# Kernel tuning notes

Measured on AMD Instinct MI355X. Metric: run time of the kernel, lower is better.

The kernel has to match this reference:

```python
import jax, jax.numpy as jnp
import numpy as np

VOCAB = 50000
EMB = 128
ENC = 128
B = 256
K = 4            # tree arity
DEPTH = 5        # root at depth 0
N_NODES = (K ** (DEPTH + 1) - 1) // (K - 1)  # 1365, BFS order: children of i are K*i+1..K*i+K


def setup_inputs() -> dict:
    key = jax.random.key(0)
    ks = jax.random.split(key, 9)
    s = 0.05
    return {
        "tokens": jax.random.randint(ks[0], (N_NODES, B), 0, VOCAB, dtype=jnp.int32),
        "emb_table": jax.random.normal(ks[1], (VOCAB, EMB), jnp.float32) * s,
        "W_ih": jax.random.normal(ks[2], (3 * ENC, EMB), jnp.float32) * s,
        "W_hh": jax.random.normal(ks[3], (3 * ENC, ENC), jnp.float32) * s,
        "b_ih": jax.random.normal(ks[4], (3 * ENC,), jnp.float32) * s,
        "b_hh": jax.random.normal(ks[5], (3 * ENC,), jnp.float32) * s,
        "sent_weight": jax.random.normal(ks[6], (ENC, ENC), jnp.float32) * s,
        "sent_bias": jax.random.normal(ks[7], (1, ENC), jnp.float32) * s,
        "context_weight": jax.random.normal(ks[8], (ENC, 1), jnp.float32) * s,
    }


def _gru_step(x, h, W_ih, W_hh, b_ih, b_hh):
    # torch.nn.GRU single step: gates ordered (r, z, n)
    gi = x @ W_ih.T + b_ih
    gh = h @ W_hh.T + b_hh
    i_r, i_z, i_n = jnp.split(gi, 3, axis=-1)
    h_r, h_z, h_n = jnp.split(gh, 3, axis=-1)
    r = jax.nn.sigmoid(i_r + h_r)
    z = jax.nn.sigmoid(i_z + h_z)
    n = jnp.tanh(i_n + r * h_n)
    return (1.0 - z) * n + z * h


def _encode(tokens, emb_table, W_ih, W_hh, b_ih, b_hh, sent_weight, sent_bias, context_weight):
    # bottom-up over levels of a full K-ary tree; vectorized over (nodes-in-level, batch)
    level_starts = [(K ** d - 1) // (K - 1) for d in range(DEPTH + 2)]
    bsz = tokens.shape[1]
    outs = []
    child_h = None  # [n_{d+1}, B, ENC] hiddens of the level below, level-local order
    for d in range(DEPTH, -1, -1):
        s, e = level_starts[d], level_starts[d + 1]
        n_d = e - s
        x = emb_table[tokens[s:e]]  # [n_d, B, EMB]
        if child_h is None:
            h0 = jnp.zeros((n_d, bsz, ENC), x.dtype)  # leaves: no children
        else:
            # children of local node j are rows j*K..j*K+K-1 of child_h
            ch = child_h.reshape(n_d, K, bsz, ENC).transpose(1, 0, 2, 3)  # [K, n_d, B, E]
            u = jnp.tanh(jnp.einsum('knbe,ef->knbf', ch, sent_weight) + sent_bias)
            scores = jnp.tanh(jnp.einsum('knbe,eo->knbo', u, context_weight))[..., 0]  # [K, n_d, B]
            alpha = jax.nn.softmax(scores, axis=0)  # softmax over children, per (node, batch)
            h0 = jnp.einsum('knbe,knb->nbe', ch, alpha)
        hn = _gru_step(x, h0, W_ih, W_hh, b_ih, b_hh)  # [n_d, B, E]
        outs.append(hn)
        child_h = hn
    all_h = jnp.concatenate(outs, axis=0)  # [N_NODES, B, E]
    return jnp.max(all_h, axis=0)  # torch.max(node_list, 0)[0]


def reference(tokens, emb_table, W_ih, W_hh, b_ih, b_hh, sent_weight, sent_bias, context_weight):
    return _encode(tokens, emb_table, W_ih, W_hh, b_ih, b_hh,
                   sent_weight, sent_bias, context_weight)
```

## Files before the change

### kernel.cpp

```cpp
#include <hip/hip_runtime.h>
#include <hip/hip_bf16.h>
#include <math.h>

typedef short s8 __attribute__((ext_vector_type(8)));
typedef float f4 __attribute__((ext_vector_type(4)));
typedef unsigned short ushort_t;

__device__ __forceinline__ float fexp2f(float x) { return __builtin_amdgcn_exp2f(x); }
__device__ __forceinline__ float frcpf(float x)  { return __builtin_amdgcn_rcpf(x); }
__device__ __forceinline__ float sigf(float x) {
    return frcpf(1.f + fexp2f(x * -1.44269504f));
}
__device__ __forceinline__ float tanh_f(float x) {
    float e = fexp2f(x * 2.88539008f);
    return 1.f - 2.f * frcpf(e + 1.f);
}
__device__ __forceinline__ unsigned pk2(float a, float b) {
    __hip_bfloat162 r = __float22bfloat162_rn(make_float2(a, b));
    return *(unsigned*)&r;
}
__device__ __forceinline__ float b2f(ushort_t b) {
    return __uint_as_float(((unsigned)b) << 16);
}

#define EMB_N   6400000
#define W_N     49152
#define SW_N    16384
#define CVT_N   (EMB_N + 2 * W_N + SW_N)

__global__ __launch_bounds__(256) void cvt_kernel(
    const float* __restrict__ emb, const float* __restrict__ wih,
    const float* __restrict__ whh, const float* __restrict__ sw,
    ushort_t* __restrict__ embb, ushort_t* __restrict__ wihb,
    ushort_t* __restrict__ whhb, ushort_t* __restrict__ swtb)
{
    int i = (blockIdx.x * 256 + threadIdx.x) * 4;
    if (i >= CVT_N) return;
    if (i < EMB_N) {
        float4 v = *(const float4*)(emb + i);
        uint2 o; o.x = pk2(v.x, v.y); o.y = pk2(v.z, v.w);
        *(uint2*)(embb + i) = o;
    } else if (i < EMB_N + W_N) {
        int j = i - EMB_N;
        float4 v = *(const float4*)(wih + j);
        uint2 o; o.x = pk2(v.x, v.y); o.y = pk2(v.z, v.w);
        *(uint2*)(wihb + j) = o;
    } else if (i < EMB_N + 2 * W_N) {
        int j = i - EMB_N - W_N;
        float4 v = *(const float4*)(whh + j);
        uint2 o; o.x = pk2(v.x, v.y); o.y = pk2(v.z, v.w);
        *(uint2*)(whhb + j) = o;
    } else {
        int j = i - EMB_N - 2 * W_N;
        int f = j >> 7, e0 = j & 127;
        uint2 o;
        o.x = pk2(sw[(e0 + 0) * 128 + f], sw[(e0 + 1) * 128 + f]);
        o.y = pk2(sw[(e0 + 2) * 128 + f], sw[(e0 + 3) * 128 + f]);
        *(uint2*)(swtb + j) = o;
    }
}

__global__ __launch_bounds__(512, 2) void leafgru_mfma(
    const ushort_t* __restrict__ embb, const ushort_t* __restrict__ wihb,
    const float* __restrict__ bih, const float* __restrict__ bhh,
    const ushort_t* __restrict__ swt, const float* __restrict__ sb,
    const float* __restrict__ cw,
    ushort_t* __restrict__ hleaf, float* __restrict__ sleaf)
{
    __shared__ ushort_t xs[128 * 136];
    __shared__ ushort_t hnew[128 * 136];
    __shared__ float scp[8][128];

    const int t = threadIdx.x;
    const int base = blockIdx.x * 128;

    {
        int lr = t >> 2, c0 = (t & 3) * 32;
        const ushort_t* src = embb + (size_t)(base + lr) * 128 + c0;
        ushort_t* dst = &xs[lr * 136 + c0];
        #pragma unroll
        for (int i = 0; i < 4; ++i) *(s8*)(dst + 8 * i) = *(const s8*)(src + 8 * i);
    }

    const int lane = t & 63, w = t >> 6;
    const int quad = lane >> 4, l15 = lane & 15;
    const int gA = w * 16 + l15;
    const int g0 = w * 16 + quad * 4;

    s8 bwi[3][4];
    #pragma unroll
    for (int gm = 0; gm < 3; ++gm) {
        const ushort_t* wp = wihb + (size_t)(gm * 128 + gA) * 128 + quad * 8;
        #pragma unroll
        for (int s = 0; s < 4; ++s) bwi[gm][s] = *(const s8*)(wp + 32 * s);
    }
    float bR[4], bZ[4], biN[4], bhN[4];
    {
        float4 a = *(const float4*)(bih + g0);
        float4 b = *(const float4*)(bhh + g0);
        bR[0] = a.x + b.x; bR[1] = a.y + b.y; bR[2] = a.z + b.z; bR[3] = a.w + b.w;
        float4 c = *(const float4*)(bih + 128 + g0);
        float4 d = *(const float4*)(bhh + 128 + g0);
        bZ[0] = c.x + d.x; bZ[1] = c.y + d.y; bZ[2] = c.z + d.z; bZ[3] = c.w + d.w;
        float4 e = *(const float4*)(bih + 256 + g0);
        float4 f = *(const float4*)(bhh + 256 + g0);
        biN[0] = e.x; biN[1] = e.y; biN[2] = e.z; biN[3] = e.w;
        bhN[0] = f.x; bhN[1] = f.y; bhN[2] = f.z; bhN[3] = f.w;
    }

    __syncthreads();

    #pragma unroll 1
    for (int mt = 0; mt < 8; ++mt) {
        const int row = mt * 16 + l15;
        s8 ax[4];
        const ushort_t* ap = &xs[row * 136 + quad * 8];
        #pragma unroll
        for (int s = 0; s < 4; ++s) ax[s] = *(const s8*)(ap + 32 * s);

        f4 accR = (f4)0.f, accZ = (f4)0.f, accN = (f4)0.f;
        #pragma unroll
        for (int s = 0; s < 4; ++s) {
            accR = __builtin_amdgcn_mfma_f32_16x16x32_bf16(bwi[0][s], ax[s], accR, 0, 0, 0);
            accZ = __builtin_amdgcn_mfma_f32_16x16x32_bf16(bwi[1][s], ax[s], accZ, 0, 0, 0);
            accN = __builtin_amdgcn_mfma_f32_16x16x32_bf16(bwi[2][s], ax[s], accN, 0, 0, 0);
        }
        float hv[4];
        #pragma unroll
        for (int r = 0; r < 4; ++r) {
            float G = fexp2f((accR[r] + bR[r]) * -1.44269504f);
            float rr = frcpf(1.f + G);
            float an = accN[r] + biN[r] + rr * bhN[r];
            float E = fexp2f(an * 2.88539008f);
            float F = fexp2f((accZ[r] + bZ[r]) * -1.44269504f);
            float d = frcpf((E + 1.f) * (1.f + F));
            hv[r] = (E - 1.f) * F * d;
        }
        uint2 ov; ov.x = pk2(hv[0], hv[1]); ov.y = pk2(hv[2], hv[3]);
        *(uint2*)&hnew[row * 136 + g0] = ov;
        *(uint2*)(hleaf + (size_t)(base + row) * 128 + g0) = ov;
    }
    __syncthreads();

    s8 bsw[4];
    {
        const ushort_t* wp = swt + (size_t)gA * 128 + quad * 8;
        #pragma unroll
        for (int s = 0; s < 4; ++s) bsw[s] = *(const s8*)(wp + 32 * s);
    }
    float sb4[4], cw4[4];
    {
        float4 a = *(const float4*)(sb + g0);
        float4 b = *(const float4*)(cw + g0);
        sb4[0] = a.x; sb4[1] = a.y; sb4[2] = a.z; sb4[3] = a.w;
        cw4[0] = b.x; cw4[1] = b.y; cw4[2] = b.z; cw4[3] = b.w;
    }

    #pragma unroll 1
    for (int mt = 0; mt < 8; ++mt) {
        const int crow = mt * 16 + l15;
        s8 a[4];
        const ushort_t* ap = &hnew[crow * 136 + quad * 8];
        #pragma unroll
        for (int s = 0; s < 4; ++s) a[s] = *(const s8*)(ap + 32 * s);

        f4 acc = (f4)0.f;
        #pragma unroll
        for (int s = 0; s < 4; ++s)
            acc = __builtin_amdgcn_mfma_f32_16x16x32_bf16(bsw[s], a[s], acc, 0, 0, 0);

        float part = 0.f;
        #pragma unroll
        for (int r = 0; r < 4; ++r)
            part += tanh_f(acc[r] + sb4[r]) * cw4[r];
        part += __shfl_xor(part, 16);
        part += __shfl_xor(part, 32);
        if (quad == 0) scp[w][crow] = part;
    }
    __syncthreads();

    if (t < 128) {
        float s = 0.f;
        #pragma unroll
        for (int ww = 0; ww < 8; ++ww) s += scp[ww][t];
        sleaf[base + t] = tanh_f(s);
    }
}

__global__ __launch_bounds__(512, 2) void gru_fused(
    const int* __restrict__ tokens, const ushort_t* __restrict__ embb,
    const ushort_t* __restrict__ hleaf, const float* __restrict__ sleaf,
    const ushort_t* __restrict__ wihb, const ushort_t* __restrict__ whhb,
    const float* __restrict__ bih, const float* __restrict__ bhh,
    ushort_t* __restrict__ hbuf, ushort_t* __restrict__ pmaxs)
{
    __shared__ ushort_t xs[128 * 136];
    __shared__ ushort_t hs[128 * 136];

    const int t = threadIdx.x;
    const int base = blockIdx.x * 128;

    {
        int rl = t >> 2, c0 = (t & 3) * 32;
        int row = base + rl;
        int node = row >> 8, b = row & 255;
        int tok = tokens[(85 + node) * 256 + b];
        const ushort_t* src = embb + (size_t)tok * 128 + c0;
        ushort_t* dst = &xs[rl * 136 + c0];
        #pragma unroll
        for (int i = 0; i < 4; ++i) *(s8*)(dst + 8 * i) = *(const s8*)(src + 8 * i);

        int lt0 = tokens[(341 + 4 * node + 0) * 256 + b];
        int lt1 = tokens[(341 + 4 * node + 1) * 256 + b];
        int lt2 = tokens[(341 + 4 * node + 2) * 256 + b];
        int lt3 = tokens[(341 + 4 * node + 3) * 256 + b];
        float s0 = sleaf[lt0], s1 = sleaf[lt1], s2 = sleaf[lt2], s3 = sleaf[lt3];
        float m = fmaxf(fmaxf(s0, s1), fmaxf(s2, s3));
        float e0 = fexp2f((s0 - m) * 1.44269504f), e1 = fexp2f((s1 - m) * 1.44269504f);
        float e2 = fexp2f((s2 - m) * 1.44269504f), e3 = fexp2f((s3 - m) * 1.44269504f);
        float inv = frcpf(e0 + e1 + e2 + e3);
        float a0 = e0 * inv, a1 = e1 * inv, a2 = e2 * inv, a3 = e3 * inv;

        const ushort_t* p0 = hleaf + (size_t)lt0 * 128 + c0;
        const ushort_t* p1 = hleaf + (size_t)lt1 * 128 + c0;
        const ushort_t* p2 = hleaf + (size_t)lt2 * 128 + c0;
        const ushort_t* p3 = hleaf + (size_t)lt3 * 128 + c0;
        ushort_t* hdst = &hs[rl * 136 + c0];
        ushort_t* pmp = pmaxs + ((size_t)b * 320 + node) * 128 + c0;
        #pragma unroll
        for (int i = 0; i < 4; ++i) {
            s8 v0 = *(const s8*)(p0 + 8 * i);
            s8 v1 = *(const s8*)(p1 + 8 * i);
            s8 v2 = *(const s8*)(p2 + 8 * i);
            s8 v3 = *(const s8*)(p3 + 8 * i);
            float o[8], mm[8];
            #pragma unroll
            for (int j = 0; j < 8; ++j) {
                float x0 = b2f((ushort_t)v0[j]), x1 = b2f((ushort_t)v1[j]);
                float x2 = b2f((ushort_t)v2[j]), x3 = b2f((ushort_t)v3[j]);
                o[j]  = a0 * x0 + a1 * x1 + a2 * x2 + a3 * x3;
                mm[j] = fmaxf(fmaxf(x0, x1), fmaxf(x2, x3));
            }
            uint4 ovv, mvv;
            ovv.x = pk2(o[0], o[1]);  ovv.y = pk2(o[2], o[3]);
            ovv.z = pk2(o[4], o[5]);  ovv.w = pk2(o[6], o[7]);
            mvv.x = pk2(mm[0], mm[1]); mvv.y = pk2(mm[2], mm[3]);
            mvv.z = pk2(mm[4], mm[5]); mvv.w = pk2(mm[6], mm[7]);
            *(uint4*)(hdst + 8 * i) = ovv;
            *(uint4*)(pmp + 8 * i)  = mvv;
        }
    }

    const int lane = t & 63, w = t >> 6;
    const int quad = lane >> 4, l15 = lane & 15;
    const int gA = w * 16 + l15;
    const int g0 = w * 16 + quad * 4;

    s8 bwi[3][4], bwh[3][4];
    #pragma unroll
    for (int gm = 0; gm < 3; ++gm) {
        const ushort_t* wp = wihb + (size_t)(gm * 128 + gA) * 128 + quad * 8;
        #pragma unroll
        for (int s = 0; s < 4; ++s) bwi[gm][s] = *(const s8*)(wp + 32 * s);
        const ushort_t* wp2 = whhb + (size_t)(gm * 128 + gA) * 128 + quad * 8;
        #pragma unroll
        for (int s = 0; s < 4; ++s) bwh[gm][s] = *(const s8*)(wp2 + 32 * s);
    }

    float bR[4], bZ[4], biN[4], bhN[4];
    {
        float4 a = *(const float4*)(bih + g0);
        float4 b = *(const float4*)(bhh + g0);
        bR[0] = a.x + b.x; bR[1] = a.y + b.y; bR[2] = a.z + b.z; bR[3] = a.w + b.w;
        float4 c = *(const float4*)(bih + 128 + g0);
        float4 d = *(const float4*)(bhh + 128 + g0);
        bZ[0] = c.x + d.x; bZ[1] = c.y + d.y; bZ[2] = c.z + d.z; bZ[3] = c.w + d.w;
        float4 e = *(const float4*)(bih + 256 + g0);
        float4 f = *(const float4*)(bhh + 256 + g0);
        biN[0] = e.x; biN[1] = e.y; biN[2] = e.z; biN[3] = e.w;
        bhN[0] = f.x; bhN[1] = f.y; bhN[2] = f.z; bhN[3] = f.w;
    }

    __syncthreads();

    #pragma unroll 1
    for (int mt = 0; mt < 8; ++mt) {
        const int row = mt * 16 + l15;
        s8 ax[4], ah[4];
        {
            const ushort_t* ap = &xs[row * 136 + quad * 8];
            #pragma unroll
            for (int s = 0; s < 4; ++s) ax[s] = *(const s8*)(ap + 32 * s);
            const ushort_t* hp = &hs[row * 136 + quad * 8];
            #pragma unroll
            for (int s = 0; s < 4; ++s) ah[s] = *(const s8*)(hp + 32 * s);
        }

        f4 accR = (f4)0.f, accZ = (f4)0.f, accN = (f4)0.f, accNh = (f4)0.f;
        #pragma unroll
        for (int s = 0; s < 4; ++s) {
            accR = __builtin_amdgcn_mfma_f32_16x16x32_bf16(bwi[0][s], ax[s], accR, 0, 0, 0);
            accZ = __builtin_amdgcn_mfma_f32_16x16x32_bf16(bwi[1][s], ax[s], accZ, 0, 0, 0);
            accN = __builtin_amdgcn_mfma_f32_16x16x32_bf16(bwi[2][s], ax[s], accN, 0, 0, 0);
        }
        #pragma unroll
        for (int s = 0; s < 4; ++s) {
            accR  = __builtin_amdgcn_mfma_f32_16x16x32_bf16(bwh[0][s], ah[s], accR, 0, 0, 0);
            accZ  = __builtin_amdgcn_mfma_f32_16x16x32_bf16(bwh[1][s], ah[s], accZ, 0, 0, 0);
            accNh = __builtin_amdgcn_mfma_f32_16x16x32_bf16(bwh[2][s], ah[s], accNh, 0, 0, 0);
        }

        float h0v[4];
        {
            short4 h04 = *(const short4*)&hs[row * 136 + g0];
            h0v[0] = b2f((ushort_t)h04.x); h0v[1] = b2f((ushort_t)h04.y);
            h0v[2] = b2f((ushort_t)h04.z); h0v[3] = b2f((ushort_t)h04.w);
        }
        float hv[4];
        #pragma unroll
        for (int r = 0; r < 4; ++r) {
            float G = fexp2f((accR[r] + bR[r]) * -1.44269504f);
            float rr = frcpf(1.f + G);
            float an = accN[r] + biN[r] + rr * (accNh[r] + bhN[r]);
            float E = fexp2f(an * 2.88539008f);
            float F = fexp2f((accZ[r] + bZ[r]) * -1.44269504f);
            float d = frcpf((E + 1.f) * (1.f + F));
            hv[r] = ((E - 1.f) * F + h0v[r] * (E + 1.f)) * d;
        }
        uint2 ov; ov.x = pk2(hv[0], hv[1]); ov.y = pk2(hv[2], hv[3]);
        *(uint2*)(hbuf + (size_t)(base + row) * 128 + g0) = ov;
    }
}

__global__ __launch_bounds__(512, 2) void attnmax_mfma(
    const ushort_t* __restrict__ hch, ushort_t* __restrict__ h0out,
    ushort_t* __restrict__ pmax,
    const ushort_t* __restrict__ swt, const float* __restrict__ sb,
    const float* __restrict__ cw)
{
    __shared__ ushort_t chs[128 * 136];
    __shared__ float scp[8][128];
    __shared__ float sc[128];
    __shared__ float al[4][32];

    const int t = threadIdx.x;
    const int pbase = blockIdx.x * 32;
    const int pnode = pbase >> 8;
    const int b0 = pbase & 255;

    {
        int lr = t >> 2, c0 = (t & 3) * 32;
        int k = lr >> 5, bl = lr & 31;
        const ushort_t* src = hch + ((size_t)(4 * pnode + k) * 256 + b0 + bl) * 128 + c0;
        ushort_t* dst = &chs[lr * 136 + c0];
        #pragma unroll
        for (int i = 0; i < 4; ++i) *(s8*)(dst + 8 * i) = *(const s8*)(src + 8 * i);
    }

    const int lane = t & 63, w = t >> 6;
    const int quad = lane >> 4, l15 = lane & 15;
    const int fA = w * 16 + l15;
    const int f0 = w * 16 + quad * 4;

    s8 bsw[4];
    {
        const ushort_t* wp = swt + (size_t)fA * 128 + quad * 8;
        #pragma unroll
        for (int s = 0; s < 4; ++s) bsw[s] = *(const s8*)(wp + 32 * s);
    }
    float sb4[4], cw4[4];
    {
        float4 a = *(const float4*)(sb + f0);
        float4 b = *(const float4*)(cw + f0);
        sb4[0] = a.x; sb4[1] = a.y; sb4[2] = a.z; sb4[3] = a.w;
        cw4[0] = b.x; cw4[1] = b.y; cw4[2] = b.z; cw4[3] = b.w;
    }
    __syncthreads();

    #pragma unroll 1
    for (int mt = 0; mt < 8; ++mt) {
        const int crow = mt * 16 + l15;
        s8 a[4];
        const ushort_t* ap = &chs[crow * 136 + quad * 8];
        #pragma unroll
        for (int s = 0; s < 4; ++s) a[s] = *(const s8*)(ap + 32 * s);

        f4 acc = (f4)0.f;
        #pragma unroll
        for (int s = 0; s < 4; ++s)
            acc = __builtin_amdgcn_mfma_f32_16x16x32_bf16(bsw[s], a[s], acc, 0, 0, 0);

        float part = 0.f;
        #pragma unroll
        for (int r = 0; r < 4; ++r)
            part += tanh_f(acc[r] + sb4[r]) * cw4[r];
        part += __shfl_xor(part, 16);
        part += __shfl_xor(part, 32);
        if (quad == 0) scp[w][crow] = part;
    }
    __syncthreads();

    if (t < 128) {
        float s = 0.f;
        #pragma unroll
        for (int ww = 0; ww < 8; ++ww) s += scp[ww][t];
        sc[t] = tanh_f(s);
    }
    __syncthreads();

    if (t < 32) {
        float s0 = sc[t], s1 = sc[32 + t], s2 = sc[64 + t], s3 = sc[96 + t];
        float m = fmaxf(fmaxf(s0, s1), fmaxf(s2, s3));
        float e0 = fexp2f((s0 - m) * 1.44269504f), e1 = fexp2f((s1 - m) * 1.44269504f);
        float e2 = fexp2f((s2 - m) * 1.44269504f), e3 = fexp2f((s3 - m) * 1.44269504f);
        float inv = frcpf(e0 + e1 + e2 + e3);
        al[0][t] = e0 * inv; al[1][t] = e1 * inv; al[2][t] = e2 * inv; al[3][t] = e3 * inv;
    }
    __syncthreads();

    {
        int bl = t >> 4, e0 = (t & 15) * 8;
        float a0 = al[0][bl], a1 = al[1][bl], a2 = al[2][bl], a3 = al[3][bl];
        s8 c0v = *(const s8*)&chs[(0 * 32 + bl) * 136 + e0];
        s8 c1v = *(const s8*)&chs[(1 * 32 + bl) * 136 + e0];
        s8 c2v = *(const s8*)&chs[(2 * 32 + bl) * 136 + e0];
        s8 c3v = *(const s8*)&chs[(3 * 32 + bl) * 136 + e0];
        float o[8], m[8];
        #pragma unroll
        for (int j = 0; j < 8; ++j) {
            float x0 = b2f((ushort_t)c0v[j]), x1 = b2f((ushort_t)c1v[j]);
            float x2 = b2f((ushort_t)c2v[j]), x3 = b2f((ushort_t)c3v[j]);
            o[j] = a0 * x0 + a1 * x1 + a2 * x2 + a3 * x3;
            m[j] = fmaxf(fmaxf(x0, x1), fmaxf(x2, x3));
        }
        uint4 ovv, mvv;
        ovv.x = pk2(o[0], o[1]); ovv.y = pk2(o[2], o[3]);
        ovv.z = pk2(o[4], o[5]); ovv.w = pk2(o[6], o[7]);
        mvv.x = pk2(m[0], m[1]); mvv.y = pk2(m[2], m[3]);
        mvv.z = pk2(m[4], m[5]); mvv.w = pk2(m[6], m[7]);
        size_t rh = ((size_t)pnode * 256 + b0 + bl) * 128 + e0;
        *(uint4*)(h0out + rh) = ovv;
        size_t rp = ((size_t)(b0 + bl) * 320 + 256 + pnode) * 128 + e0;
        *(uint4*)(pmax + rp) = mvv;
    }
}

__global__ __launch_bounds__(512, 1) void tail_kernel(
    const int* __restrict__ tokens, const ushort_t* __restrict__ embb,
    const ushort_t* __restrict__ wihb, const ushort_t* __restrict__ whhb,
    const float* __restrict__ bih, const float* __restrict__ bhh,
    const ushort_t* __restrict__ swt, const float* __restrict__ sb,
    const float* __restrict__ cw,
    const ushort_t* __restrict__ h0g,
    const ushort_t* __restrict__ pmax,
    float* __restrict__ out)
{
    __shared__ ushort_t xs[64 * 136];
    __shared__ ushort_t hnew[64 * 136];
    __shared__ ushort_t hs[64 * 136];
    __shared__ float scp[8][64];
    __shared__ float sc[64];
    __shared__ float al[4][16];
    __shared__ float smax[4][128];
    __shared__ float wpart[8][128];

    const int t = threadIdx.x;
    const int bb = blockIdx.x;
    const int lane = t & 63, w = t >> 6;
    const int quad = lane >> 4, l15 = lane & 15;
    const int gA = w * 16 + l15;
    const int g0 = w * 16 + quad * 4;

    s8 bwi[3][4], bwh[3][4];
    #pragma unroll
    for (int gm = 0; gm < 3; ++gm) {
        const ushort_t* wp = wihb + (size_t)(gm * 128 + gA) * 128 + quad * 8;
        #pragma unroll
        for (int s = 0; s < 4; ++s) bwi[gm][s] = *(const s8*)(wp + 32 * s);
        const ushort_t* wp2 = whhb + (size_t)(gm * 128 + gA) * 128 + quad * 8;
        #pragma unroll
        for (int s = 0; s < 4; ++s) bwh[gm][s] = *(const s8*)(wp2 + 32 * s);
    }
    float bR[4], bZ[4], biN[4], bhN[4];
    {
        float4 a = *(const float4*)(bih + g0);
        float4 b = *(const float4*)(bhh + g0);
        bR[0] = a.x + b.x; bR[1] = a.y + b.y; bR[2] = a.z + b.z; bR[3] = a.w + b.w;
        float4 c = *(const float4*)(bih + 128 + g0);
        float4 d = *(const float4*)(bhh + 128 + g0);
        bZ[0] = c.x + d.x; bZ[1] = c.y + d.y; bZ[2] = c.z + d.z; bZ[3] = c.w + d.w;
        float4 e = *(const float4*)(bih + 256 + g0);
        float4 f = *(const float4*)(bhh + 256 + g0);
        biN[0] = e.x; biN[1] = e.y; biN[2] = e.z; biN[3] = e.w;
        bhN[0] = f.x; bhN[1] = f.y; bhN[2] = f.z; bhN[3] = f.w;
    }
    s8 bsw[4];
    {
        const ushort_t* wp = swt + (size_t)gA * 128 + quad * 8;
        #pragma unroll
        for (int s = 0; s < 4; ++s) bsw[s] = *(const s8*)(wp + 32 * s);
    }
    float sb4[4], cw4[4];
    {
        float4 a = *(const float4*)(sb + g0);
        float4 b = *(const float4*)(cw + g0);
        sb4[0] = a.x; sb4[1] = a.y; sb4[2] = a.z; sb4[3] = a.w;
        cw4[0] = b.x; cw4[1] = b.y; cw4[2] = b.z; cw4[3] = b.w;
    }

    float vmax = -INFINITY;

    const int nodesA[4] = {64, 16, 4, 1};
    const int tok0A[4]  = {21, 5, 1, 0};

    #pragma unroll 1
    for (int L = 0; L < 4; ++L) {
        const int nodes = nodesA[L], tok0 = tok0A[L];
        const int R = (nodes < 16) ? 16 : nodes;
        const int mts = R >> 4;

        {
            int lr = t >> 3, c0 = (t & 7) * 16;
            if (lr < R) {
                int n = min(lr, nodes - 1);
                int tok = tokens[(tok0 + n) * 256 + bb];
                const ushort_t* src = embb + (size_t)tok * 128 + c0;
                ushort_t* dst = &xs[lr * 136 + c0];
                *(s8*)(dst)     = *(const s8*)(src);
                *(s8*)(dst + 8) = *(const s8*)(src + 8);
                if (L == 0) {
                    const ushort_t* hsrc = h0g + ((size_t)n * 256 + bb) * 128 + c0;
                    ushort_t* hdst = &hs[lr * 136 + c0];
                    *(s8*)(hdst)     = *(const s8*)(hsrc);
                    *(s8*)(hdst + 8) = *(const s8*)(hsrc + 8);
                }
            }
        }
        __syncthreads();

        for (int mt = 0; mt < mts; ++mt) {
            const int row = mt * 16 + l15;
            const int hr = min(row, nodes - 1);
            s8 ax[4], ah[4];
            {
                const ushort_t* ap = &xs[row * 136 + quad * 8];
                #pragma unroll
                for (int s = 0; s < 4; ++s) ax[s] = *(const s8*)(ap + 32 * s);
                const ushort_t* hp = &hs[hr * 136 + quad * 8];
                #pragma unroll
                for (int s = 0; s < 4; ++s) ah[s] = *(const s8*)(hp + 32 * s);
            }
            f4 accR = (f4)0.f, accZ = (f4)0.f, accN = (f4)0.f, accNh = (f4)0.f;
            #pragma unroll
            for (int s = 0; s < 4; ++s) {
                accR = __builtin_amdgcn_mfma_f32_16x16x32_bf16(bwi[0][s], ax[s], accR, 0, 0, 0);
                accZ = __builtin_amdgcn_mfma_f32_16x16x32_bf16(bwi[1][s], ax[s], accZ, 0, 0, 0);
                accN = __builtin_amdgcn_mfma_f32_16x16x32_bf16(bwi[2][s], ax[s], accN, 0, 0, 0);
            }
            #pragma unroll
            for (int s = 0; s < 4; ++s) {
                accR  = __builtin_amdgcn_mfma_f32_16x16x32_bf16(bwh[0][s], ah[s], accR, 0, 0, 0);
                accZ  = __builtin_amdgcn_mfma_f32_16x16x32_bf16(bwh[1][s], ah[s], accZ, 0, 0, 0);
                accNh = __builtin_amdgcn_mfma_f32_16x16x32_bf16(bwh[2][s], ah[s], accNh, 0, 0, 0);
            }
            float h0v[4];
            {
                short4 h04 = *(const short4*)&hs[hr * 136 + g0];
                h0v[0] = b2f((ushort_t)h04.x); h0v[1] = b2f((ushort_t)h04.y);
                h0v[2] = b2f((ushort_t)h04.z); h0v[3] = b2f((ushort_t)h04.w);
            }
            float hv[4];
            #pragma unroll
            for (int r = 0; r < 4; ++r) {
                float rr = sigf(accR[r] + bR[r]);
                float zz = sigf(accZ[r] + bZ[r]);
                float nn = tanh_f(accN[r] + biN[r] + rr * (accNh[r] + bhN[r]));
                hv[r] = nn + zz * (h0v[r] - nn);
            }
            uint2 ov; ov.x = pk2(hv[0], hv[1]); ov.y = pk2(hv[2], hv[3]);
            *(uint2*)&hnew[row * 136 + g0] = ov;
        }
        __syncthreads();

        {
            int col = t & 127, g = t >> 7;
            for (int r = g; r < R; r += 4)
                vmax = fmaxf(vmax, b2f(hnew[r * 136 + col]));
        }

        if (L < 3) {
            for (int mt = 0; mt < mts; ++mt) {
                const int crow = mt * 16 + l15;
                s8 a[4];
                const ushort_t* ap = &hnew[crow * 136 + quad * 8];
                #pragma unroll
                for (int s = 0; s < 4; ++s) a[s] = *(const s8*)(ap + 32 * s);
                f4 acc = (f4)0.f;
                #pragma unroll
                for (int s = 0; s < 4; ++s)
                    acc = __builtin_amdgcn_mfma_f32_16x16x32_bf16(bsw[s], a[s], acc, 0, 0, 0);
                float part = 0.f;
                #pragma unroll
                for (int r = 0; r < 4; ++r)
                    part += tanh_f(acc[r] + sb4[r]) * cw4[r];
                part += __shfl_xor(part, 16);
                part += __shfl_xor(part, 32);
                if (quad == 0) scp[w][crow] = part;
            }
            __syncthreads();
            if (t < R) {
                float s = 0.f;
                #pragma unroll
                for (int g = 0; g < 8; ++g) s += scp[g][t];
                sc[t] = tanh_f(s);
            }
            __syncthreads();
            const int P = nodes >> 2;
            if (t < P) {
                float s0 = sc[4 * t + 0], s1 = sc[4 * t + 1];
                float s2 = sc[4 * t + 2], s3 = sc[4 * t + 3];
                float m = fmaxf(fmaxf(s0, s1), fmaxf(s2, s3));
                float e0 = fexp2f((s0 - m) * 1.44269504f);
                float e1 = fexp2f((s1 - m) * 1.44269504f);
                float e2 = fexp2f((s2 - m) * 1.44269504f);
                float e3 = fexp2f((s3 - m) * 1.44269504f);
                float inv = frcpf(e0 + e1 + e2 + e3);
                al[0][t] = e0 * inv; al[1][t] = e1 * inv;
                al[2][t] = e2 * inv; al[3][t] = e3 * inv;
            }
            __syncthreads();
            if (t < 16 * P) {
                int bl = t >> 4, e0 = (t & 15) * 8;
                float a0 = al[0][bl], a1 = al[1][bl], a2 = al[2][bl], a3 = al[3][bl];
                s8 c0v = *(const s8*)&hnew[(4 * bl + 0) * 136 + e0];
                s8 c1v = *(const s8*)&hnew[(4 * bl + 1) * 136 + e0];
                s8 c2v = *(const s8*)&hnew[(4 * bl + 2) * 136 + e0];
                s8 c3v = *(const s8*)&hnew[(4 * bl + 3) * 136 + e0];
                float o[8];
                #pragma unroll
                for (int j = 0; j < 8; ++j) {
                    o[j] = a0 * b2f((ushort_t)c0v[j]) + a1 * b2f((ushort_t)c1v[j])
                         + a2 * b2f((ushort_t)c2v[j]) + a3 * b2f((ushort_t)c3v[j]);
                }
                uint4 ovv;
                ovv.x = pk2(o[0], o[1]); ovv.y = pk2(o[2], o[3]);
                ovv.z = pk2(o[4], o[5]); ovv.w = pk2(o[6], o[7]);
                *(uint4*)&hs[bl * 136 + e0] = ovv;
            }
            __syncthreads();
        }
    }

    smax[t >> 7][t & 127] = vmax;

    {
        int cg = t & 15;
        int ck = t >> 4;
        const ushort_t* base = pmax + (size_t)bb * 320 * 128 + cg * 8;
        float v8[8];
        #pragma unroll
        for (int j = 0; j < 8; ++j) v8[j] = -INFINITY;
        for (int s = ck; s < 320; s += 32) {
            s8 c = *(const s8*)(base + (size_t)s * 128);
            #pragma unroll
            for (int j = 0; j < 8; ++j) v8[j] = fmaxf(v8[j], b2f((ushort_t)c[j]));
        }
        #pragma unroll
        for (int j = 0; j < 8; ++j) {
            v8[j] = fmaxf(v8[j], __shfl_xor(v8[j], 16));
            v8[j] = fmaxf(v8[j], __shfl_xor(v8[j], 32));
        }
        if (lane < 16) {
            #pragma unroll
            for (int j = 0; j < 8; ++j) wpart[w][lane * 8 + j] = v8[j];
        }
    }
    __syncthreads();

    if (t < 128) {
        float m = wpart[0][t];
        #pragma unroll
        for (int ww = 1; ww < 8; ++ww) m = fmaxf(m, wpart[ww][t]);
        float own = fmaxf(fmaxf(smax[0][t], smax[1][t]),
                          fmaxf(smax[2][t], smax[3][t]));
        out[(size_t)bb * 128 + t] = fmaxf(m, own);
    }
}

extern "C" void kernel_launch(void* const* d_in, const int* in_sizes, int n_in,
                              void* d_out, int out_size, void* d_ws, size_t ws_size,
                              hipStream_t stream)
{
    const int*   tokens = (const int*)d_in[0];
    const float* emb    = (const float*)d_in[1];
    const float* Wih    = (const float*)d_in[2];
    const float* Whh    = (const float*)d_in[3];
    const float* bih    = (const float*)d_in[4];
    const float* bhh    = (const float*)d_in[5];
    const float* SW     = (const float*)d_in[6];
    const float* sb     = (const float*)d_in[7];
    const float* cw     = (const float*)d_in[8];
    float* out = (float*)d_out;

    ushort_t* embb  = (ushort_t*)d_ws;
    ushort_t* wihb  = embb + (size_t)EMB_N;
    ushort_t* whhb  = wihb + W_N;
    ushort_t* swtb  = whhb + W_N;
    ushort_t* hleaf = swtb + SW_N;
    float*    sleaf = (float*)(hleaf + (size_t)50176 * 128);
    ushort_t* h4    = (ushort_t*)(sleaf + 50176);
    ushort_t* h0_3  = h4 + (size_t)256 * 32768;
    ushort_t* pmax  = h0_3 + (size_t)64 * 32768;

    cvt_kernel<<<(CVT_N / 4 + 255) / 256, 256, 0, stream>>>(
        emb, Wih, Whh, SW, embb, wihb, whhb, swtb);

    leafgru_mfma<<<392, 512, 0, stream>>>(
        embb, wihb, bih, bhh, swtb, sb, cw, hleaf, sleaf);

    gru_fused<<<512, 512, 0, stream>>>(
        tokens, embb, hleaf, sleaf, wihb, whhb, bih, bhh, h4, pmax);

    attnmax_mfma<<<512, 512, 0, stream>>>(h4, h0_3, pmax, swtb, sb, cw);

    tail_kernel<<<256, 512, 0, stream>>>(
        tokens, embb, wihb, whhb, bih, bhh, swtb, sb, cw,
        h0_3, pmax, out);
}
```

Baseline: 184.6 us.

## Pipeline leaf gather with MFMA GRU compute in level-4 fused kernel

The 128-row tile load (embedding rows, leaf hiddens, leaf scores) is split into four 32-row stages. The loads for the next stage are issued before computing the current two 16-row MFMA tiles, and that stage is finished into shared memory afterwards. This is meant to hide gather latency behind matrix work instead of doing all loads up front. It adds a __syncthreads per stage and keeps prefetched registers live, which raises register pressure.

Measured after the change: 181.8 us. Within noise of the previous version (-1.5%).

```diff
diff --git a/kernel.cpp b/kernel.cpp
--- a/kernel.cpp
+++ b/kernel.cpp
@@ -200,62 +200,14 @@
     const int t = threadIdx.x;
     const int base = blockIdx.x * 128;
 
-    {
-        int rl = t >> 2, c0 = (t & 3) * 32;
-        int row = base + rl;
-        int node = row >> 8, b = row & 255;
-        int tok = tokens[(85 + node) * 256 + b];
-        const ushort_t* src = embb + (size_t)tok * 128 + c0;
-        ushort_t* dst = &xs[rl * 136 + c0];
-        #pragma unroll
-        for (int i = 0; i < 4; ++i) *(s8*)(dst + 8 * i) = *(const s8*)(src + 8 * i);
-
-        int lt0 = tokens[(341 + 4 * node + 0) * 256 + b];
-        int lt1 = tokens[(341 + 4 * node + 1) * 256 + b];
-        int lt2 = tokens[(341 + 4 * node + 2) * 256 + b];
-        int lt3 = tokens[(341 + 4 * node + 3) * 256 + b];
-        float s0 = sleaf[lt0], s1 = sleaf[lt1], s2 = sleaf[lt2], s3 = sleaf[lt3];
-        float m = fmaxf(fmaxf(s0, s1), fmaxf(s2, s3));
-        float e0 = fexp2f((s0 - m) * 1.44269504f), e1 = fexp2f((s1 - m) * 1.44269504f);
-        float e2 = fexp2f((s2 - m) * 1.44269504f), e3 = fexp2f((s3 - m) * 1.44269504f);
-        float inv = frcpf(e0 + e1 + e2 + e3);
-        float a0 = e0 * inv, a1 = e1 * inv, a2 = e2 * inv, a3 = e3 * inv;
-
-        const ushort_t* p0 = hleaf + (size_t)lt0 * 128 + c0;
-        const ushort_t* p1 = hleaf + (size_t)lt1 * 128 + c0;
-        const ushort_t* p2 = hleaf + (size_t)lt2 * 128 + c0;
-        const ushort_t* p3 = hleaf + (size_t)lt3 * 128 + c0;
-        ushort_t* hdst = &hs[rl * 136 + c0];
-        ushort_t* pmp = pmaxs + ((size_t)b * 320 + node) * 128 + c0;
-        #pragma unroll
-        for (int i = 0; i < 4; ++i) {
-            s8 v0 = *(const s8*)(p0 + 8 * i);
-            s8 v1 = *(const s8*)(p1 + 8 * i);
-            s8 v2 = *(const s8*)(p2 + 8 * i);
-            s8 v3 = *(const s8*)(p3 + 8 * i);
-            float o[8], mm[8];
-            #pragma unroll
-            for (int j = 0; j < 8; ++j) {
-                float x0 = b2f((ushort_t)v0[j]), x1 = b2f((ushort_t)v1[j]);
-                float x2 = b2f((ushort_t)v2[j]), x3 = b2f((ushort_t)v3[j]);
-                o[j]  = a0 * x0 + a1 * x1 + a2 * x2 + a3 * x3;
-                mm[j] = fmaxf(fmaxf(x0, x1), fmaxf(x2, x3));
-            }
-            uint4 ovv, mvv;
-            ovv.x = pk2(o[0], o[1]);  ovv.y = pk2(o[2], o[3]);
-            ovv.z = pk2(o[4], o[5]);  ovv.w = pk2(o[6], o[7]);
-            mvv.x = pk2(mm[0], mm[1]); mvv.y = pk2(mm[2], mm[3]);
-            mvv.z = pk2(mm[4], mm[5]); mvv.w = pk2(mm[6], mm[7]);
-            *(uint4*)(hdst + 8 * i) = ovv;
-            *(uint4*)(pmp + 8 * i)  = mvv;
-        }
-    }
-
     const int lane = t & 63, w = t >> 6;
     const int quad = lane >> 4, l15 = lane & 15;
     const int gA = w * 16 + l15;
     const int g0 = w * 16 + quad * 4;
 
+    const int slr = t >> 4;
+    const int sc0 = (t & 15) * 8;
+
     s8 bwi[3][4], bwh[3][4];
     #pragma unroll
     for (int gm = 0; gm < 3; ++gm) {
@@ -266,7 +218,6 @@
         #pragma unroll
         for (int s = 0; s < 4; ++s) bwh[gm][s] = *(const s8*)(wp2 + 32 * s);
     }
-
     float bR[4], bZ[4], biN[4], bhN[4];
     {
         float4 a = *(const float4*)(bih + g0);
@@ -281,55 +232,117 @@
         bhN[0] = f.x; bhN[1] = f.y; bhN[2] = f.z; bhN[3] = f.w;
     }
 
+    s8 pv0, pv1, pv2, pv3, pxv;
+    float ps0, ps1, ps2, ps3;
+    int pnode, pb;
+
+#define STAGE_LOAD(Q) {                                                     \
+        int lr_ = (Q) * 32 + slr;                                           \
+        int grow_ = base + lr_;                                             \
+        pnode = grow_ >> 8; pb = grow_ & 255;                               \
+        int lt0 = tokens[(341 + 4 * pnode + 0) * 256 + pb];                 \
+        int lt1 = tokens[(341 + 4 * pnode + 1) * 256 + pb];                 \
+        int lt2 = tokens[(341 + 4 * pnode + 2) * 256 + pb];                 \
+        int lt3 = tokens[(341 + 4 * pnode + 3) * 256 + pb];                 \
+        pv0 = *(const s8*)(hleaf + (size_t)lt0 * 128 + sc0);                \
+        pv1 = *(const s8*)(hleaf + (size_t)lt1 * 128 + sc0);                \
+        pv2 = *(const s8*)(hleaf + (size_t)lt2 * 128 + sc0);                \
+        pv3 = *(const s8*)(hleaf + (size_t)lt3 * 128 + sc0);                \
+        ps0 = sleaf[lt0]; ps1 = sleaf[lt1]; ps2 = sleaf[lt2]; ps3 = sleaf[lt3]; \
+        int tok_ = tokens[(85 + pnode) * 256 + pb];                         \
+        pxv = *(const s8*)(embb + (size_t)tok_ * 128 + sc0);                \
+    }
+
+#define STAGE_FIN(Q) {                                                      \
+        int lr_ = (Q) * 32 + slr;                                           \
+        float m_ = fmaxf(fmaxf(ps0, ps1), fmaxf(ps2, ps3));                 \
+        float e0_ = fexp2f((ps0 - m_) * 1.44269504f);                       \
+        float e1_ = fexp2f((ps1 - m_) * 1.44269504f);                       \
+        float e2_ = fexp2f((ps2 - m_) * 1.44269504f);                       \
+        float e3_ = fexp2f((ps3 - m_) * 1.44269504f);                       \
+        float inv_ = frcpf(e0_ + e1_ + e2_ + e3_);                          \
+        float a0_ = e0_ * inv_, a1_ = e1_ * inv_;                           \
+        float a2_ = e2_ * inv_, a3_ = e3_ * inv_;                           \
+        float o_[8], mm_[8];                                                \
+        _Pragma("unroll")                                                   \
+        for (int j = 0; j < 8; ++j) {                                       \
+            float y0 = b2f((ushort_t)pv0[j]), y1 = b2f((ushort_t)pv1[j]);   \
+            float y2 = b2f((ushort_t)pv2[j]), y3 = b2f((ushort_t)pv3[j]);   \
+            o_[j]  = a0_ * y0 + a1_ * y1 + a2_ * y2 + a3_ * y3;             \
+            mm_[j] = fmaxf(fmaxf(y0, y1), fmaxf(y2, y3));                   \
+        }                                                                   \
+        uint4 ovv_, mvv_;                                                   \
+        ovv_.x = pk2(o_[0], o_[1]);  ovv_.y = pk2(o_[2], o_[3]);            \
+        ovv_.z = pk2(o_[4], o_[5]);  ovv_.w = pk2(o_[6], o_[7]);            \
+        mvv_.x = pk2(mm_[0], mm_[1]); mvv_.y = pk2(mm_[2], mm_[3]);         \
+        mvv_.z = pk2(mm_[4], mm_[5]); mvv_.w = pk2(mm_[6], mm_[7]);         \
+        *(uint4*)&hs[lr_ * 136 + sc0] = ovv_;                               \
+        *(s8*)&xs[lr_ * 136 + sc0] = pxv;                                   \
+        *(uint4*)(pmaxs + ((size_t)pb * 320 + pnode) * 128 + sc0) = mvv_;   \
+    }
+
+    STAGE_LOAD(0);
+    STAGE_FIN(0);
     __syncthreads();
 
     #pragma unroll 1
-    for (int mt = 0; mt < 8; ++mt) {
-        const int row = mt * 16 + l15;
-        s8 ax[4], ah[4];
-        {
-            const ushort_t* ap = &xs[row * 136 + quad * 8];
+    for (int q = 0; q < 4; ++q) {
+        if (q < 3) STAGE_LOAD(q + 1);
+
+        #pragma unroll 1
+        for (int mq = 0; mq < 2; ++mq) {
+            const int mt = q * 2 + mq;
+            const int row = mt * 16 + l15;
+            s8 ax[4], ah[4];
+            {
+                const ushort_t* ap = &xs[row * 136 + quad * 8];
+                #pragma unroll
+                for (int s = 0; s < 4; ++s) ax[s] = *(const s8*)(ap + 32 * s);
+                const ushort_t* hp = &hs[row * 136 + quad * 8];
+                #pragma unroll
+                for (int s = 0; s < 4; ++s) ah[s] = *(const s8*)(hp + 32 * s);
+            }
+
+            f4 accR = (f4)0.f, accZ = (f4)0.f, accN = (f4)0.f, accNh = (f4)0.f;
             #pragma unroll
-            for (int s = 0; s < 4; ++s) ax[s] = *(const s8*)(ap + 32 * s);
-            const ushort_t* hp = &hs[row * 136 + quad * 8];
+            for (int s = 0; s < 4; ++s) {
+                accR = __builtin_amdgcn_mfma_f32_16x16x32_bf16(bwi[0][s], ax[s], accR, 0, 0, 0);
+                accZ = __builtin_amdgcn_mfma_f32_16x16x32_bf16(bwi[1][s], ax[s], accZ, 0, 0, 0);
+                accN = __builtin_amdgcn_mfma_f32_16x16x32_bf16(bwi[2][s], ax[s], accN, 0, 0, 0);
+            }
             #pragma unroll
-            for (int s = 0; s < 4; ++s) ah[s] = *(const s8*)(hp + 32 * s);
-        }
-
-        f4 accR = (f4)0.f, accZ = (f4)0.f, accN = (f4)0.f, accNh = (f4)0.f;
-        #pragma unroll
-        for (int s = 0; s < 4; ++s) {
-            accR = __builtin_amdgcn_mfma_f32_16x16x32_bf16(bwi[0][s], ax[s], accR, 0, 0, 0);
-            accZ = __builtin_amdgcn_mfma_f32_16x16x32_bf16(bwi[1][s], ax[s], accZ, 0, 0, 0);
-            accN = __builtin_amdgcn_mfma_f32_16x16x32_bf16(bwi[2][s], ax[s], accN, 0, 0, 0);
-        }
-        #pragma unroll
-        for (int s = 0; s < 4; ++s) {
-            accR  = __builtin_amdgcn_mfma_f32_16x16x32_bf16(bwh[0][s], ah[s], accR, 0, 0, 0);
-            accZ  = __builtin_amdgcn_mfma_f32_16x16x32_bf16(bwh[1][s], ah[s], accZ, 0, 0, 0);
-            accNh = __builtin_amdgcn_mfma_f32_16x16x32_bf16(bwh[2][s], ah[s], accNh, 0, 0, 0);
-        }
-
-        float h0v[4];
-        {
-            short4 h04 = *(const short4*)&hs[row * 136 + g0];
-            h0v[0] = b2f((ushort_t)h04.x); h0v[1] = b2f((ushort_t)h04.y);
-            h0v[2] = b2f((ushort_t)h04.z); h0v[3] = b2f((ushort_t)h04.w);
-        }
-        float hv[4];
-        #pragma unroll
-        for (int r = 0; r < 4; ++r) {
-            float G = fexp2f((accR[r] + bR[r]) * -1.44269504f);
-            float rr = frcpf(1.f + G);
-            float an = accN[r] + biN[r] + rr * (accNh[r] + bhN[r]);
-            float E = fexp2f(an * 2.88539008f);
-            float F = fexp2f((accZ[r] + bZ[r]) * -1.44269504f);
-            float d = frcpf((E + 1.f) * (1.f + F));
-            hv[r] = ((E - 1.f) * F + h0v[r] * (E + 1.f)) * d;
-        }
-        uint2 ov; ov.x = pk2(hv[0], hv[1]); ov.y = pk2(hv[2], hv[3]);
-        *(uint2*)(hbuf + (size_t)(base + row) * 128 + g0) = ov;
-    }
+            for (int s = 0; s < 4; ++s) {
+                accR  = __builtin_amdgcn_mfma_f32_16x16x32_bf16(bwh[0][s], ah[s], accR, 0, 0, 0);
+                accZ  = __builtin_amdgcn_mfma_f32_16x16x32_bf16(bwh[1][s], ah[s], accZ, 0, 0, 0);
+                accNh = __builtin_amdgcn_mfma_f32_16x16x32_bf16(bwh[2][s], ah[s], accNh, 0, 0, 0);
+            }
+
+            float h0v[4];
+            {
+                short4 h04 = *(const short4*)&hs[row * 136 + g0];
+                h0v[0] = b2f((ushort_t)h04.x); h0v[1] = b2f((ushort_t)h04.y);
+                h0v[2] = b2f((ushort_t)h04.z); h0v[3] = b2f((ushort_t)h04.w);
+            }
+            float hv[4];
+            #pragma unroll
+            for (int r = 0; r < 4; ++r) {
+                float G = fexp2f((accR[r] + bR[r]) * -1.44269504f);
+                float rr = frcpf(1.f + G);
+                float an = accN[r] + biN[r] + rr * (accNh[r] + bhN[r]);
+                float E = fexp2f(an * 2.88539008f);
+                float F = fexp2f((accZ[r] + bZ[r]) * -1.44269504f);
+                float d = frcpf((E + 1.f) * (1.f + F));
+                hv[r] = ((E - 1.f) * F + h0v[r] * (E + 1.f)) * d;
+            }
+            uint2 ov; ov.x = pk2(hv[0], hv[1]); ov.y = pk2(hv[2], hv[3]);
+            *(uint2*)(hbuf + (size_t)(base + row) * 128 + g0) = ov;
+        }
+
+        if (q < 3) STAGE_FIN(q + 1);
+        __syncthreads();
+    }
+#undef STAGE_LOAD
+#undef STAGE_FIN
 }
 
 __global__ __launch_bounds__(512, 2) void attnmax_mfma(
```
